# Kernel optimization log

Measured on AMD Instinct MI355X. Metric: run time of the kernel, lower is better.

Reference implementation:

```python
import jax, jax.numpy as jnp
import numpy as np

DIM = 64
N_GRAPHS = 300
N_NODES = 12000
N_EDGES = 40000


def setup_inputs() -> dict:
    key = jax.random.key(0)
    ks = jax.random.split(key, 16)
    N, E, F_IN, D = N_NODES, N_EDGES, 14, DIM

    def w(k, shape, fan_in):
        return jax.random.normal(k, shape, dtype=jnp.float32) / np.float32(np.sqrt(fan_in))

    return {
        "x": jax.random.normal(ks[0], (N, F_IN), dtype=jnp.float32),
        "edge_index": jax.random.randint(ks[1], (2, E), 0, N),
        "edge_attr": jax.random.uniform(ks[2], (E, 4), dtype=jnp.float32),
        "batch": jnp.sort(jax.random.randint(ks[3], (N,), 0, N_GRAPHS)),
        # lin0
        "lin0_w": w(ks[4], (D, F_IN), F_IN), "lin0_b": jnp.zeros((D,), jnp.float32),
        # edge MLP: Linear(4,128) -> ReLU -> Linear(128, D*D)
        "nn1_w": w(ks[5], (128, 4), 4), "nn1_b": jnp.zeros((128,), jnp.float32),
        "nn2_w": w(ks[6], (D * D, 128), 128), "nn2_b": jnp.zeros((D * D,), jnp.float32),
        # NNConv root weight + bias
        "root_w": w(ks[7], (D, D), D), "conv_b": jnp.zeros((D,), jnp.float32),
        # GRU(D, D), gate order r,z,n
        "gru_w_ih": w(ks[8], (3 * D, D), D), "gru_w_hh": w(ks[9], (3 * D, D), D),
        "gru_b_ih": jnp.zeros((3 * D,), jnp.float32), "gru_b_hh": jnp.zeros((3 * D,), jnp.float32),
        # Set2Set LSTM(2D -> D), gate order i,f,g,o
        "lstm_w_ih": w(ks[10], (4 * D, 2 * D), 2 * D), "lstm_w_hh": w(ks[11], (4 * D, D), D),
        "lstm_b_ih": jnp.zeros((4 * D,), jnp.float32), "lstm_b_hh": jnp.zeros((4 * D,), jnp.float32),
        # readout
        "lin1_w": w(ks[12], (D, 2 * D), 2 * D), "lin1_b": jnp.zeros((D,), jnp.float32),
        "lin2_w": w(ks[13], (1, D), D), "lin2_b": jnp.zeros((1,), jnp.float32),
    }


def _mpnn_forward(x, edge_index, edge_attr, batch,
                  lin0_w, lin0_b, nn1_w, nn1_b, nn2_w, nn2_b, root_w, conv_b,
                  gru_w_ih, gru_w_hh, gru_b_ih, gru_b_hh,
                  lstm_w_ih, lstm_w_hh, lstm_b_ih, lstm_b_hh,
                  lin1_w, lin1_b, lin2_w, lin2_b):
    N, D, B = x.shape[0], DIM, N_GRAPHS
    src, dst = edge_index[0], edge_index[1]

    out = jax.nn.relu(x @ lin0_w.T + lin0_b)          # [N, D]
    h = out

    # per-edge weight matrices from edge MLP: [E, D, D]
    W_e = (jax.nn.relu(edge_attr @ nn1_w.T + nn1_b) @ nn2_w.T + nn2_b).reshape(-1, D, D)
    deg = jnp.maximum(
        jax.ops.segment_sum(jnp.ones(src.shape, x.dtype), dst, num_segments=N), 1.0)

    for _ in range(3):
        # NNConv: gather -> per-edge bmm -> scatter-mean, plus root term and bias
        msg = jnp.einsum('ei,eio->eo', out[src], W_e)                 # [E, D]
        agg = jax.ops.segment_sum(msg, dst, num_segments=N) / deg[:, None]
        m = jax.nn.relu(out @ root_w + agg + conv_b)
        # GRU cell (torch gate order r, z, n)
        gx = m @ gru_w_ih.T + gru_b_ih
        gh = h @ gru_w_hh.T + gru_b_hh
        r = jax.nn.sigmoid(gx[:, :D] + gh[:, :D])
        z = jax.nn.sigmoid(gx[:, D:2 * D] + gh[:, D:2 * D])
        n = jnp.tanh(gx[:, 2 * D:] + r * gh[:, 2 * D:])
        h = (1.0 - z) * n + z * h
        out = h

    per_atom_out = out

    # Set2Set pooling, 3 processing steps
    q_star = jnp.zeros((B, 2 * D), x.dtype)
    hs = jnp.zeros((B, D), x.dtype)
    cs = jnp.zeros((B, D), x.dtype)
    for _ in range(3):
        gates = q_star @ lstm_w_ih.T + lstm_b_ih + hs @ lstm_w_hh.T + lstm_b_hh
        i_g = jax.nn.sigmoid(gates[:, 0 * D:1 * D])
        f_g = jax.nn.sigmoid(gates[:, 1 * D:2 * D])
        g_g = jnp.tanh(gates[:, 2 * D:3 * D])
        o_g = jax.nn.sigmoid(gates[:, 3 * D:4 * D])
        cs = f_g * cs + i_g * g_g
        hs = o_g * jnp.tanh(cs)
        q = hs                                                         # [B, D]
        e = jnp.sum(out * q[batch], axis=-1)                           # [N]
        e_max = jax.ops.segment_max(e, batch, num_segments=B)
        a = jnp.exp(e - e_max[batch])
        a = a / jax.ops.segment_sum(a, batch, num_segments=B)[batch]   # scatter-softmax
        r_read = jax.ops.segment_sum(a[:, None] * out, batch, num_segments=B)
        q_star = jnp.concatenate([q, r_read], axis=-1)                 # [B, 2D]

    y = jax.nn.relu(q_star @ lin1_w.T + lin1_b)
    y = (y @ lin2_w.T + lin2_b).reshape(-1)                            # [B]
    return (y, per_atom_out)


def reference(x, edge_index, edge_attr, batch,
              lin0_w, lin0_b, nn1_w, nn1_b, nn2_w, nn2_b, root_w, conv_b,
              gru_w_ih, gru_w_hh, gru_b_ih, gru_b_hh,
              lstm_w_ih, lstm_w_hh, lstm_b_ih, lstm_b_hh,
              lin1_w, lin1_b, lin2_w, lin2_b):
    return _mpnn_forward(x, edge_index, edge_attr, batch,
                         lin0_w, lin0_b, nn1_w, nn1_b, nn2_w, nn2_b, root_w, conv_b,
                         gru_w_ih, gru_w_hh, gru_b_ih, gru_b_hh,
                         lstm_w_ih, lstm_w_hh, lstm_b_ih, lstm_b_hh,
                         lin1_w, lin1_b, lin2_w, lin2_b)
```

## Files before the change

kernel.cpp:

```cpp
#include <hip/hip_runtime.h>
#include <math.h>

#define NBG 300
#define KP 8256

typedef __attribute__((ext_vector_type(8))) short short8_t;
typedef __attribute__((ext_vector_type(4))) float f32x4_t;

#define MFMA16(a,b,c) __builtin_amdgcn_mfma_f32_16x16x32_bf16(a,b,c,0,0,0)

__device__ __forceinline__ float sigmoidf_(float x){ return 1.0f/(1.0f+expf(-x)); }
__device__ __forceinline__ float bf2f(short s){
  union{unsigned u; float f;} v; v.u = ((unsigned)(unsigned short)s) << 16; return v.f;
}
__device__ __forceinline__ short f2bf(float f){
  union{float f; unsigned u;} v; v.f = f;
  unsigned r = (v.u + 0x7fffu + ((v.u >> 16) & 1u)) >> 16;
  return (short)r;
}
__device__ __forceinline__ unsigned cvt_pk_bf16(float lo, float hi){
  unsigned r;
  asm volatile("v_cvt_pk_bf16_f32 %0, %1, %2" : "=v"(r) : "v"(lo), "v"(hi));
  return r;
}
union FragA { short8_t v; unsigned u[4]; };

__device__ __forceinline__ short8_t frag_from(float sv, short8_t h){
  union { short8_t v; unsigned u[4]; } hh; hh.v = h;
  FragA fa;
  #pragma unroll
  for (int k2 = 0; k2 < 4; ++k2){
    float lo = __uint_as_float(hh.u[k2] << 16);
    float hi = __uint_as_float(hh.u[k2] & 0xffff0000u);
    fa.u[k2] = cvt_pk_bf16(sv*lo, sv*hi);
  }
  return fa.v;
}

__global__ void lin0_kernel(const float* __restrict__ x, const float* __restrict__ w,
                            const float* __restrict__ b, float* __restrict__ out,
                            short* __restrict__ out_bf, int N){
  int n = blockIdx.x; int d = threadIdx.x;
  __shared__ float xs[16];
  if (d < 14) xs[d] = x[n*14 + d];
  __syncthreads();
  float acc = b[d];
  #pragma unroll
  for (int k = 0; k < 14; ++k) acc = fmaf(xs[k], w[d*14 + k], acc);
  float v = fmaxf(acc, 0.0f);
  out[n*64 + d] = v;
  out_bf[n*64 + d] = f2bf(v);
}

__global__ void ehid_kernel(const float* __restrict__ ea, const float* __restrict__ w,
                            const float* __restrict__ b, short* __restrict__ hid_bf, int E){
  int e = blockIdx.x; int t = threadIdx.x;
  __shared__ float as[4];
  if (t < 4) as[t] = ea[e*4 + t];
  __syncthreads();
  float acc = b[t];
  #pragma unroll
  for (int k = 0; k < 4; ++k) acc = fmaf(as[k], w[t*4 + k], acc);
  hid_bf[(size_t)e*128 + t] = f2bf(fmaxf(acc, 0.0f));
}

__global__ void count_kernel(const int* __restrict__ idx, int* __restrict__ counts, int len){
  int e = blockIdx.x*blockDim.x + threadIdx.x;
  if (e < len) atomicAdd(&counts[idx[e]], 1);
}

__global__ __launch_bounds__(1024) void scan_kernel(const int* __restrict__ counts,
    int* __restrict__ starts, int* __restrict__ cursor, int N){
  __shared__ int part[1024];
  int t = threadIdx.x;
  int per = (N + 1023) >> 10;
  int base = t * per;
  int s = 0;
  for (int j = 0; j < per; ++j){ int idx = base + j; if (idx < N) s += counts[idx]; }
  part[t] = s;
  __syncthreads();
  for (int off = 1; off < 1024; off <<= 1){
    int v = (t >= off) ? part[t - off] : 0;
    __syncthreads();
    part[t] += v;
    __syncthreads();
  }
  int run = (t == 0) ? 0 : part[t-1];
  for (int j = 0; j < per; ++j){
    int idx = base + j;
    if (idx < N){ starts[idx] = run; cursor[idx] = run; run += counts[idx]; }
  }
}

__global__ void scatter_kernel(const int* __restrict__ dst, int* __restrict__ cursor,
                               int* __restrict__ sorted_eid, int E){
  int e = blockIdx.x*blockDim.x + threadIdx.x;
  if (e < E){ int p = atomicAdd(&cursor[dst[e]], 1); sorted_eid[p] = e; }
}

__global__ void w2t_build(const float* __restrict__ w2, const float* __restrict__ b2,
                          short* __restrict__ W2t){
  int o = blockIdx.x;
  for (int k = threadIdx.x; k < KP; k += blockDim.x){
    float val;
    if (k < 8192){ int i = k >> 7, h = k & 127; val = w2[(size_t)(i*64 + o)*128 + h]; }
    else val = b2[(k - 8192)*64 + o];
    W2t[(size_t)o*KP + k] = f2bf(val);
  }
}

__global__ __launch_bounds__(256) void msg_gemm3(
    const short* __restrict__ out_bf, const short* __restrict__ hid_bf,
    const short* __restrict__ W2t, const int* __restrict__ sorted,
    const int* __restrict__ src, const int* __restrict__ dstv,
    float* __restrict__ agg, int E)
{
  __shared__ short sSb[128*80];
  __shared__ __align__(16) char bufB[4][4096];
  __shared__ int eid_s[128];
  __shared__ int dst_s[128];

  const int tid = threadIdx.x;
  const int blk = blockIdx.x;
  const int split = blockIdx.y;

  if (tid < 128){
    int p = blk*128 + tid;
    int e = (p < E) ? sorted[p] : -1;
    eid_s[tid] = e;
    dst_s[tid] = (e >= 0) ? dstv[e] : -1;
  }
  __syncthreads();

  const int lane = tid & 63, wid = tid >> 6;
  const int r = lane & 15, q4 = lane >> 4;
  const int eloc0 = wid*32 + r;
  const int eloc1 = eloc0 + 16;

  short8_t z8 = {0,0,0,0,0,0,0,0};

  {
    int row = tid >> 1, half = tid & 1;
    int e = eid_s[row];
    short* dp = sSb + row*80 + half*32;
    if (e >= 0){
      const short* sp = out_bf + (size_t)src[e]*64 + half*32;
      *(short8_t*)(dp)      = *(const short8_t*)(sp);
      *(short8_t*)(dp + 8)  = *(const short8_t*)(sp + 8);
      *(short8_t*)(dp + 16) = *(const short8_t*)(sp + 16);
      *(short8_t*)(dp + 24) = *(const short8_t*)(sp + 24);
    } else {
      *(short8_t*)(dp) = z8; *(short8_t*)(dp + 8) = z8;
      *(short8_t*)(dp + 16) = z8; *(short8_t*)(dp + 24) = z8;
    }
  }

  short8_t hq0_0=z8, hq0_1=z8, hq0_2=z8, hq0_3=z8;
  short8_t hq1_0=z8, hq1_1=z8, hq1_2=z8, hq1_3=z8;
  {
    int e0 = eid_s[eloc0], e1 = eid_s[eloc1];
    if (e0 >= 0){
      const short* hp = hid_bf + (size_t)e0*128 + q4*8;
      hq0_0 = *(const short8_t*)(hp);      hq0_1 = *(const short8_t*)(hp + 32);
      hq0_2 = *(const short8_t*)(hp + 64); hq0_3 = *(const short8_t*)(hp + 96);
    }
    if (e1 >= 0){
      const short* hp = hid_bf + (size_t)e1*128 + q4*8;
      hq1_0 = *(const short8_t*)(hp);      hq1_1 = *(const short8_t*)(hp + 32);
      hq1_2 = *(const short8_t*)(hp + 64); hq1_3 = *(const short8_t*)(hp + 96);
    }
  }

  const int gl_o  = tid >> 2;
  const int gl_kq = (tid & 3) ^ ((tid >> 3) & 3);
  const char* w2b = (const char*)W2t;
  const size_t gbase = (size_t)gl_o*(KP*2) + (size_t)gl_kq*16;

  int boff0, boff1, boff2, boff3;
  {
    int o0 = r, o1 = 16 + r, o2 = 32 + r, o3 = 48 + r;
    boff0 = (o0*4 + (q4 ^ ((o0 >> 1) & 3))) * 16;
    boff1 = (o1*4 + (q4 ^ ((o1 >> 1) & 3))) * 16;
    boff2 = (o2*4 + (q4 ^ ((o2 >> 1) & 3))) * 16;
    boff3 = (o3*4 + (q4 ^ ((o3 >> 1) & 3))) * 16;
  }

  const int nc     = split ? 130 : 128;
  const int cstart = split * 128;
  const int clast  = cstart + nc - 1;

#define GLOAD(c_, bi_)                                                          \
  __builtin_amdgcn_global_load_lds(                                             \
      (const __attribute__((address_space(1))) unsigned*)(w2b + gbase + (size_t)(c_)*64), \
      (__attribute__((address_space(3))) unsigned*)(&bufB[bi_][wid*1024]), 16, 0, 0)

  GLOAD(cstart + 0, (cstart + 0) & 3);
  GLOAD(cstart + 1, (cstart + 1) & 3);
  GLOAD(cstart + 2, (cstart + 2) & 3);
  __syncthreads();

  f32x4_t zz = {0.f,0.f,0.f,0.f};
  f32x4_t acc00 = zz, acc01 = zz, acc02 = zz, acc03 = zz;
  f32x4_t acc10 = zz, acc11 = zz, acc12 = zz, acc13 = zz;

#define CHUNK(QI, Q, HQ0, HQ1)                                                  \
  {                                                                             \
    int c = cstart + (QI)*4 + (Q);                                              \
    asm volatile("s_waitcnt vmcnt(2) lgkmcnt(0)" ::: "memory");                 \
    __builtin_amdgcn_s_barrier();                                               \
    const char* bp = bufB[c & 3];                                               \
    short8_t b0 = *(const short8_t*)(bp + boff0);                               \
    short8_t b1 = *(const short8_t*)(bp + boff1);                               \
    short8_t b2 = *(const short8_t*)(bp + boff2);                               \
    short8_t b3 = *(const short8_t*)(bp + boff3);                               \
    { int cn = c + 3; if (cn > clast) cn = clast; GLOAD(cn, (c + 3) & 3); }     \
    short8_t f0 = frag_from(sv0, HQ0);                                          \
    short8_t f1 = frag_from(sv1, HQ1);                                          \
    acc00 = MFMA16(f0, b0, acc00);                                              \
    acc01 = MFMA16(f0, b1, acc01);                                              \
    acc02 = MFMA16(f0, b2, acc02);                                              \
    acc03 = MFMA16(f0, b3, acc03);                                              \
    acc10 = MFMA16(f1, b0, acc10);                                              \
    acc11 = MFMA16(f1, b1, acc11);                                              \
    acc12 = MFMA16(f1, b2, acc12);                                              \
    acc13 = MFMA16(f1, b3, acc13);                                              \
  }

  #pragma unroll 1
  for (int qi = 0; qi < 32; ++qi){
    int qg = (split << 5) + qi;
    float sv0 = bf2f(sSb[eloc0*80 + qg]);
    float sv1 = bf2f(sSb[eloc1*80 + qg]);
    CHUNK(qi, 0, hq0_0, hq1_0)
    CHUNK(qi, 1, hq0_1, hq1_1)
    CHUNK(qi, 2, hq0_2, hq1_2)
    CHUNK(qi, 3, hq0_3, hq1_3)
  }

  if (split){
    #pragma unroll
    for (int tc = 0; tc < 2; ++tc){
      int c = 256 + tc;
      asm volatile("s_waitcnt vmcnt(2) lgkmcnt(0)" ::: "memory");
      __builtin_amdgcn_s_barrier();
      const char* bp = bufB[c & 3];
      short8_t b0 = *(const short8_t*)(bp + boff0);
      short8_t b1 = *(const short8_t*)(bp + boff1);
      short8_t b2 = *(const short8_t*)(bp + boff2);
      short8_t b3 = *(const short8_t*)(bp + boff3);
      GLOAD(clast, (c + 3) & 3);
      short8_t f0 = *(const short8_t*)(sSb + eloc0*80 + tc*32 + q4*8);
      short8_t f1 = *(const short8_t*)(sSb + eloc1*80 + tc*32 + q4*8);
      acc00 = MFMA16(f0, b0, acc00);
      acc01 = MFMA16(f0, b1, acc01);
      acc02 = MFMA16(f0, b2, acc02);
      acc03 = MFMA16(f0, b3, acc03);
      acc10 = MFMA16(f1, b0, acc10);
      acc11 = MFMA16(f1, b1, acc11);
      acc12 = MFMA16(f1, b2, acc12);
      acc13 = MFMA16(f1, b3, acc13);
    }
  }

  asm volatile("s_waitcnt vmcnt(0)" ::: "memory");

  {
    int ebase = wid*32 + q4*4;
    float c0 = 0.f, c1 = 0.f, c2 = 0.f, c3 = 0.f;
    #pragma unroll
    for (int reg = 0; reg < 4; ++reg){
      c0 += acc00[reg]; c1 += acc01[reg]; c2 += acc02[reg]; c3 += acc03[reg];
      int d = dst_s[ebase + reg];
      int dn = (reg < 3) ? dst_s[ebase + reg + 1] : -2;
      if (d != dn){
        if (d >= 0){
          float* ap = agg + (size_t)d*64;
          atomicAdd(ap + r,      c0);
          atomicAdd(ap + 16 + r, c1);
          atomicAdd(ap + 32 + r, c2);
          atomicAdd(ap + 48 + r, c3);
        }
        c0 = c1 = c2 = c3 = 0.f;
      }
    }
  }
  {
    int ebase = wid*32 + 16 + q4*4;
    float c0 = 0.f, c1 = 0.f, c2 = 0.f, c3 = 0.f;
    #pragma unroll
    for (int reg = 0; reg < 4; ++reg){
      c0 += acc10[reg]; c1 += acc11[reg]; c2 += acc12[reg]; c3 += acc13[reg];
      int d = dst_s[ebase + reg];
      int dn = (reg < 3) ? dst_s[ebase + reg + 1] : -2;
      if (d != dn){
        if (d >= 0){
          float* ap = agg + (size_t)d*64;
          atomicAdd(ap + r,      c0);
          atomicAdd(ap + 16 + r, c1);
          atomicAdd(ap + 32 + r, c2);
          atomicAdd(ap + 48 + r, c3);
        }
        c0 = c1 = c2 = c3 = 0.f;
      }
    }
  }
#undef CHUNK
#undef GLOAD
}

__global__ __launch_bounds__(256) void node_mfma(
    const short* __restrict__ out_bf, const float* __restrict__ agg,
    const int* __restrict__ counts,
    const float* __restrict__ root_w, const float* __restrict__ conv_b,
    const float* __restrict__ gwih, const float* __restrict__ gwhh,
    const float* __restrict__ gbih, const float* __restrict__ gbhh,
    float* __restrict__ out, short* __restrict__ out_bf_w,
    float* __restrict__ out_dup, int N)
{
  __shared__ short XH[64*128];
  __shared__ short rootT[64*64];
  __shared__ short Wih_s[192*64];
  __shared__ short Whh_s[192*64];
  __shared__ float rdeg_s[64];
  __shared__ float cb_s[64];

  int tid = threadIdx.x;
  int blk = blockIdx.x;
  int nbase = blk*64;

  {
    int n = tid >> 2, cq = tid & 3;
    int ng = nbase + n;
    short8_t v0 = {0,0,0,0,0,0,0,0}, v1 = v0;
    if (ng < N){
      const short* p = out_bf + (size_t)ng*64;
      v0 = *(const short8_t*)(p + cq*16);
      v1 = *(const short8_t*)(p + cq*16 + 8);
    }
    int c0 = 8 + cq*2;
    *(short8_t*)(XH + n*128 + ((c0     ^ (n & 7))*8)) = v0;
    *(short8_t*)(XH + n*128 + (((c0+1) ^ (n & 7))*8)) = v1;
  }
  {
    int i = tid >> 2, dq = tid & 3;
    #pragma unroll
    for (int j = 0; j < 16; ++j){
      int d = dq*16 + j;
      short v = f2bf(root_w[i*64 + d]);
      rootT[d*64 + (((i >> 3) ^ (d & 7))*8) + (i & 7)] = v;
    }
  }
  if (tid < 192){
    int g = tid;
    short pk[8];
    #pragma unroll
    for (int c = 0; c < 8; ++c){
      #pragma unroll
      for (int j = 0; j < 8; ++j) pk[j] = f2bf(gwih[g*64 + c*8 + j]);
      *(short8_t*)(Wih_s + g*64 + ((c ^ (g & 7))*8)) = *(short8_t*)&pk[0];
    }
    #pragma unroll
    for (int c = 0; c < 8; ++c){
      #pragma unroll
      for (int j = 0; j < 8; ++j) pk[j] = f2bf(gwhh[g*64 + c*8 + j]);
      *(short8_t*)(Whh_s + g*64 + ((c ^ (g & 7))*8)) = *(short8_t*)&pk[0];
    }
  }
  if (tid < 64){
    int ng = nbase + tid;
    int c = (ng < N) ? counts[ng] : 1;
    rdeg_s[tid] = 1.0f / fmaxf((float)c, 1.0f);
    cb_s[tid] = conv_b[tid];
  }
  __syncthreads();

  int lane = tid & 63, wid = tid >> 6;
  int r = lane & 15, q4 = lane >> 4;

  {
    int mh = (wid >> 1)*32, nh = (wid & 1)*32;
    f32x4_t z4 = {0.f,0.f,0.f,0.f};
    f32x4_t c00 = z4, c01 = z4, c10 = z4, c11 = z4;
    #pragma unroll
    for (int ks = 0; ks < 2; ++ks){
      int ck = 8 + ks*4 + q4;
      int swA = (ck ^ (r & 7))*8;
      int swB = ((ks*4 + q4) ^ (r & 7))*8;
      short8_t a0 = *(const short8_t*)(XH + (mh + r)*128 + swA);
      short8_t a1 = *(const short8_t*)(XH + (mh + 16 + r)*128 + swA);
      short8_t b0 = *(const short8_t*)(rootT + (nh + r)*64 + swB);
      short8_t b1 = *(const short8_t*)(rootT + (nh + 16 + r)*64 + swB);
      c00 = MFMA16(a0, b0, c00);
      c01 = MFMA16(a0, b1, c01);
      c10 = MFMA16(a1, b0, c10);
      c11 = MFMA16(a1, b1, c11);
    }
    #pragma unroll
    for (int mm = 0; mm < 2; ++mm){
      #pragma unroll
      for (int nn = 0; nn < 2; ++nn){
        f32x4_t cc = mm == 0 ? (nn == 0 ? c00 : c01) : (nn == 0 ? c10 : c11);
        int d = nh + nn*16 + r;
        #pragma unroll
        for (int reg = 0; reg < 4; ++reg){
          int n = mh + mm*16 + q4*4 + reg;
          int ng = nbase + n;
          float av = (ng < N) ? agg[(size_t)ng*64 + d] : 0.0f;
          float v = cc[reg] + av * rdeg_s[n] + cb_s[d];
          v = fmaxf(v, 0.0f);
          XH[n*128 + (((d >> 3) ^ (n & 7))*8) + (d & 7)] = f2bf(v);
        }
      }
    }
  }
  __syncthreads();

  f32x4_t ax[4][3], ah[4][3];
  {
    f32x4_t z4 = {0.f,0.f,0.f,0.f};
    #pragma unroll
    for (int mt = 0; mt < 4; ++mt)
      #pragma unroll
      for (int gt = 0; gt < 3; ++gt){ ax[mt][gt] = z4; ah[mt][gt] = z4; }
  }
  #pragma unroll
  for (int ks = 0; ks < 2; ++ks){
    int ckM = ks*4 + q4;
    int ckH = 8 + ks*4 + q4;
    int swM = (ckM ^ (r & 7))*8;
    int swH = (ckH ^ (r & 7))*8;
    int swB = ((ks*4 + q4) ^ (r & 7))*8;
    short8_t bx[3], bh[3];
    #pragma unroll
    for (int gt = 0; gt < 3; ++gt){
      int g = gt*64 + wid*16 + r;
      bx[gt] = *(const short8_t*)(Wih_s + g*64 + swB);
      bh[gt] = *(const short8_t*)(Whh_s + g*64 + swB);
    }
    #pragma unroll
    for (int mt = 0; mt < 4; ++mt){
      short8_t aM = *(const short8_t*)(XH + (mt*16 + r)*128 + swM);
      short8_t aH = *(const short8_t*)(XH + (mt*16 + r)*128 + swH);
      #pragma unroll
      for (int gt = 0; gt < 3; ++gt){
        ax[mt][gt] = MFMA16(aM, bx[gt], ax[mt][gt]);
        ah[mt][gt] = MFMA16(aH, bh[gt], ah[mt][gt]);
      }
    }
  }

  {
    int d = wid*16 + r;
    float bir = gbih[d],      bhr = gbhh[d];
    float biz = gbih[64 + d], bhz = gbhh[64 + d];
    float bin_ = gbih[128 + d], bhn = gbhh[128 + d];
    #pragma unroll
    for (int mt = 0; mt < 4; ++mt){
      #pragma unroll
      for (int reg = 0; reg < 4; ++reg){
        int n = mt*16 + q4*4 + reg;
        int ng = nbase + n;
        if (ng < N){
          float gxr = ax[mt][0][reg], gxz = ax[mt][1][reg], gxn = ax[mt][2][reg];
          float ghr = ah[mt][0][reg], ghz = ah[mt][1][reg], ghn = ah[mt][2][reg];
          float rr = sigmoidf_(gxr + ghr + bir + bhr);
          float zz = sigmoidf_(gxz + ghz + biz + bhz);
          float nn = tanhf(gxn + bin_ + rr*(ghn + bhn));
          float h = out[(size_t)ng*64 + d];
          float v = (1.0f - zz)*nn + zz*h;
          out[(size_t)ng*64 + d] = v;
          out_bf_w[(size_t)ng*64 + d] = f2bf(v);
          if (out_dup) out_dup[(size_t)ng*64 + d] = v;
        }
      }
    }
  }
}

__global__ __launch_bounds__(256) void set2set_kernel(
    const float* __restrict__ out, const int* __restrict__ bstarts,
    const int* __restrict__ bcounts,
    const float* __restrict__ lwih, const float* __restrict__ lwhh,
    const float* __restrict__ lbih, const float* __restrict__ lbhh,
    const float* __restrict__ l1w, const float* __restrict__ l1b,
    const float* __restrict__ l2w, const float* __restrict__ l2b,
    float* __restrict__ y)
{
  int b = blockIdx.x, t = threadIdx.x;
  int lane = t & 63, wid = t >> 6;
  __shared__ float qs[128];
  __shared__ float hsl[64], hs_s[64], cs_s[64];
  __shared__ float ev[512];
  __shared__ float red[256];
  __shared__ float rpart[4][64];
  __shared__ float scal[2];

  int s0 = bstarts[b], cnt = bcounts[b];
  if (cnt > 512) cnt = 512;
  if (t < 64){ hs_s[t] = 0.f; cs_s[t] = 0.f; }
  if (t < 128) qs[t] = 0.f;
  __syncthreads();

  for (int step = 0; step < 3; ++step){
    if (t < 64) hsl[t] = hs_s[t];
    __syncthreads();
    {
      float a0 = lbih[t] + lbhh[t], a1 = 0.f, a2 = 0.f, a3 = 0.f;
      const float* wi = lwih + t*128;
      #pragma unroll
      for (int kq = 0; kq < 32; ++kq){
        float4 w4 = *(const float4*)(wi + kq*4);
        a0 = fmaf(qs[kq*4+0], w4.x, a0);
        a1 = fmaf(qs[kq*4+1], w4.y, a1);
        a2 = fmaf(qs[kq*4+2], w4.z, a2);
        a3 = fmaf(qs[kq*4+3], w4.w, a3);
      }
      const float* wh = lwhh + t*64;
      #pragma unroll
      for (int kq = 0; kq < 16; ++kq){
        float4 w4 = *(const float4*)(wh + kq*4);
        a0 = fmaf(hsl[kq*4+0], w4.x, a0);
        a1 = fmaf(hsl[kq*4+1], w4.y, a1);
        a2 = fmaf(hsl[kq*4+2], w4.z, a2);
        a3 = fmaf(hsl[kq*4+3], w4.w, a3);
      }
      red[t] = (a0 + a1) + (a2 + a3);
    }
    __syncthreads();
    if (t < 64){
      float ig = sigmoidf_(red[t]);
      float fg = sigmoidf_(red[64 + t]);
      float gg = tanhf(red[128 + t]);
      float og = sigmoidf_(red[192 + t]);
      float c = fg*cs_s[t] + ig*gg;
      cs_s[t] = c;
      hs_s[t] = og*tanhf(c);
    }
    __syncthreads();

    float lmax = -1e30f;
    for (int idx = t; idx < cnt; idx += 256){
      const float* row = out + (size_t)(s0 + idx)*64;
      float a0 = 0.f, a1 = 0.f, a2 = 0.f, a3 = 0.f;
      #pragma unroll
      for (int kq = 0; kq < 16; ++kq){
        float4 v = *(const float4*)(row + kq*4);
        a0 = fmaf(v.x, hs_s[kq*4+0], a0);
        a1 = fmaf(v.y, hs_s[kq*4+1], a1);
        a2 = fmaf(v.z, hs_s[kq*4+2], a2);
        a3 = fmaf(v.w, hs_s[kq*4+3], a3);
      }
      float acc = (a0 + a1) + (a2 + a3);
      ev[idx] = acc;
      lmax = fmaxf(lmax, acc);
    }
    red[t] = lmax;
    __syncthreads();
    #pragma unroll
    for (int off = 128; off > 0; off >>= 1){
      if (t < off) red[t] = fmaxf(red[t], red[t + off]);
      __syncthreads();
    }
    if (t == 0) scal[0] = red[0];
    __syncthreads();
    float m = scal[0];

    float ls = 0.f;
    for (int idx = t; idx < cnt; idx += 256){
      float a = expf(ev[idx] - m);
      ev[idx] = a;
      ls += a;
    }
    red[t] = ls;
    __syncthreads();
    #pragma unroll
    for (int off = 128; off > 0; off >>= 1){
      if (t < off) red[t] += red[t + off];
      __syncthreads();
    }
    if (t == 0) scal[1] = red[0];
    __syncthreads();
    float lst = scal[1];

    float part = 0.f;
    for (int idx = wid; idx < cnt; idx += 4)
      part = fmaf(ev[idx], out[(size_t)(s0 + idx)*64 + lane], part);
    rpart[wid][lane] = part;
    __syncthreads();
    if (t < 64){
      float r = (rpart[0][t] + rpart[1][t]) + (rpart[2][t] + rpart[3][t]);
      r = (cnt > 0) ? r / lst : 0.f;
      qs[t] = hs_s[t];
      qs[64 + t] = r;
    }
    __syncthreads();
  }

  if (t < 64){
    float a0 = l1b[t], a1 = 0.f, a2 = 0.f, a3 = 0.f;
    const float* w1 = l1w + t*128;
    #pragma unroll
    for (int kq = 0; kq < 32; ++kq){
      float4 w4 = *(const float4*)(w1 + kq*4);
      a0 = fmaf(qs[kq*4+0], w4.x, a0);
      a1 = fmaf(qs[kq*4+1], w4.y, a1);
      a2 = fmaf(qs[kq*4+2], w4.z, a2);
      a3 = fmaf(qs[kq*4+3], w4.w, a3);
    }
    float acc = (a0 + a1) + (a2 + a3);
    float v = fmaxf(acc, 0.0f) * l2w[t];
    #pragma unroll
    for (int off = 32; off > 0; off >>= 1) v += __shfl_xor(v, off, 64);
    if (t == 0) y[b] = v + l2b[0];
  }
}

extern "C" void kernel_launch(void* const* d_in, const int* in_sizes, int n_in,
                              void* d_out, int out_size, void* d_ws, size_t ws_size,
                              hipStream_t stream){
  const float* x      = (const float*)d_in[0];
  const int*   ei     = (const int*)  d_in[1];
  const float* ea     = (const float*)d_in[2];
  const int*   batch  = (const int*)  d_in[3];
  const float* lin0_w = (const float*)d_in[4];
  const float* lin0_b = (const float*)d_in[5];
  const float* nn1_w  = (const float*)d_in[6];
  const float* nn1_b  = (const float*)d_in[7];
  const float* nn2_w  = (const float*)d_in[8];
  const float* nn2_b  = (const float*)d_in[9];
  const float* root_w = (const float*)d_in[10];
  const float* conv_b = (const float*)d_in[11];
  const float* gwih   = (const float*)d_in[12];
  const float* gwhh   = (const float*)d_in[13];
  const float* gbih   = (const float*)d_in[14];
  const float* gbhh   = (const float*)d_in[15];
  const float* lwih   = (const float*)d_in[16];
  const float* lwhh   = (const float*)d_in[17];
  const float* lbih   = (const float*)d_in[18];
  const float* lbhh   = (const float*)d_in[19];
  const float* l1w    = (const float*)d_in[20];
  const float* l1b    = (const float*)d_in[21];
  const float* l2w    = (const float*)d_in[22];
  const float* l2b    = (const float*)d_in[23];

  const int N = in_sizes[0] / 14;
  const int E = in_sizes[1] / 2;
  const int B = NBG;
  const int* src  = ei;
  const int* dstv = ei + E;

  char* wsp = (char*)d_ws; size_t off = 0;
  auto alloc = [&](size_t bytes)->char* {
    char* p = wsp + off; off += (bytes + 255) & ~((size_t)255); return p;
  };
  float* out     = (float*)alloc((size_t)N*64*4);
  short* out_bf  = (short*)alloc((size_t)N*64*2);
  float* agg     = (float*)alloc((size_t)N*64*4);
  int*   counts  = (int*)  alloc((size_t)N*4);
  int*   starts  = (int*)  alloc((size_t)N*4);
  int*   cursor  = (int*)  alloc((size_t)N*4);
  int*   sorted  = (int*)  alloc((size_t)E*4);
  int*   bcounts = (int*)  alloc((size_t)B*4);
  int*   bstarts = (int*)  alloc((size_t)B*4);
  int*   bcursor = (int*)  alloc((size_t)B*4);
  short* hid_bf  = (short*)alloc((size_t)E*128*2);
  short* W2t     = (short*)alloc((size_t)64*KP*2);

  lin0_kernel<<<N, 64, 0, stream>>>(x, lin0_w, lin0_b, out, out_bf, N);
  ehid_kernel<<<E, 128, 0, stream>>>(ea, nn1_w, nn1_b, hid_bf, E);

  hipMemsetAsync(counts, 0, (size_t)N*4, stream);
  count_kernel<<<(E + 255)/256, 256, 0, stream>>>(dstv, counts, E);
  scan_kernel<<<1, 1024, 0, stream>>>(counts, starts, cursor, N);
  scatter_kernel<<<(E + 255)/256, 256, 0, stream>>>(dstv, cursor, sorted, E);

  hipMemsetAsync(bcounts, 0, (size_t)B*4, stream);
  count_kernel<<<(N + 255)/256, 256, 0, stream>>>(batch, bcounts, N);
  scan_kernel<<<1, 1024, 0, stream>>>(bcounts, bstarts, bcursor, B);

  w2t_build<<<64, 256, 0, stream>>>(nn2_w, nn2_b, W2t);

  int mblocks = (E + 127)/128;
  int nblocks = (N + 63)/64;
  dim3 mg(mblocks, 2);
  for (int it = 0; it < 3; ++it){
    hipMemsetAsync(agg, 0, (size_t)N*64*4, stream);
    msg_gemm3<<<mg, 256, 0, stream>>>(out_bf, hid_bf, W2t, sorted, src, dstv, agg, E);
    node_mfma<<<nblocks, 256, 0, stream>>>(out_bf, agg, counts, root_w, conv_b,
                                           gwih, gwhh, gbih, gbhh, out, out_bf,
                                           (it == 2) ? ((float*)d_out + 300) : nullptr, N);
  }

  set2set_kernel<<<B, 256, 0, stream>>>(out, bstarts, bcounts, lwih, lwhh, lbih, lbhh,
                                        l1w, l1b, l2w, l2b, (float*)d_out);
}
```

Before: 388.6 us.

## Deepen msg GEMM prefetch pipeline, fuse count/scan launches, zero agg in consumer

The message GEMM now keeps eight LDS stages of W2 tiles instead of four and handles two K-chunks per barrier, which halves the barrier count and keeps more global loads in flight. The A-tile row padding also shrinks from 80 to 72 shorts. The two count kernels and the two scan kernels are each merged into one launch, sharing a single memset over contiguous buffers. The per-iteration agg memset is replaced by node_mfma zeroing agg after it reads it. In exchange, LDS use grows and the wait counts in the tail path depend on the exact prefetch bookkeeping.

```diff
diff --git a/kernel.cpp b/kernel.cpp
--- a/kernel.cpp
+++ b/kernel.cpp
@@ -64,13 +64,22 @@
   hid_bf[(size_t)e*128 + t] = f2bf(fmaxf(acc, 0.0f));
 }
 
-__global__ void count_kernel(const int* __restrict__ idx, int* __restrict__ counts, int len){
-  int e = blockIdx.x*blockDim.x + threadIdx.x;
-  if (e < len) atomicAdd(&counts[idx[e]], 1);
-}
-
-__global__ __launch_bounds__(1024) void scan_kernel(const int* __restrict__ counts,
-    int* __restrict__ starts, int* __restrict__ cursor, int N){
+__global__ void count2_kernel(const int* __restrict__ dstv, int E,
+                              const int* __restrict__ batch, int N,
+                              int* __restrict__ counts, int* __restrict__ bcounts){
+  int i = blockIdx.x*blockDim.x + threadIdx.x;
+  if (i < E) atomicAdd(&counts[dstv[i]], 1);
+  int j = i - E;
+  if (j >= 0 && j < N) atomicAdd(&bcounts[batch[j]], 1);
+}
+
+__global__ __launch_bounds__(1024) void scan2_kernel(
+    const int* __restrict__ countsA, int* __restrict__ startsA, int* __restrict__ cursorA, int NA,
+    const int* __restrict__ countsB, int* __restrict__ startsB, int* __restrict__ cursorB, int NB){
+  const int* counts = blockIdx.x ? countsB : countsA;
+  int* starts = blockIdx.x ? startsB : startsA;
+  int* cursor = blockIdx.x ? cursorB : cursorA;
+  int N = blockIdx.x ? NB : NA;
   __shared__ int part[1024];
   int t = threadIdx.x;
   int per = (N + 1023) >> 10;
@@ -109,14 +118,14 @@
   }
 }
 
-__global__ __launch_bounds__(256) void msg_gemm3(
+__global__ __launch_bounds__(256) void msg_gemm4(
     const short* __restrict__ out_bf, const short* __restrict__ hid_bf,
     const short* __restrict__ W2t, const int* __restrict__ sorted,
     const int* __restrict__ src, const int* __restrict__ dstv,
     float* __restrict__ agg, int E)
 {
-  __shared__ short sSb[128*80];
-  __shared__ __align__(16) char bufB[4][4096];
+  __shared__ short sSb[128*72];
+  __shared__ __align__(16) char bufB[8][4096];
   __shared__ int eid_s[128];
   __shared__ int dst_s[128];
 
@@ -142,7 +151,7 @@
   {
     int row = tid >> 1, half = tid & 1;
     int e = eid_s[row];
-    short* dp = sSb + row*80 + half*32;
+    short* dp = sSb + row*72 + half*32;
     if (e >= 0){
       const short* sp = out_bf + (size_t)src[e]*64 + half*32;
       *(short8_t*)(dp)      = *(const short8_t*)(sp);
@@ -194,72 +203,95 @@
       (const __attribute__((address_space(1))) unsigned*)(w2b + gbase + (size_t)(c_)*64), \
       (__attribute__((address_space(3))) unsigned*)(&bufB[bi_][wid*1024]), 16, 0, 0)
 
-  GLOAD(cstart + 0, (cstart + 0) & 3);
-  GLOAD(cstart + 1, (cstart + 1) & 3);
-  GLOAD(cstart + 2, (cstart + 2) & 3);
-  __syncthreads();
+  GLOAD(cstart + 0, 0); GLOAD(cstart + 1, 1); GLOAD(cstart + 2, 2);
+  GLOAD(cstart + 3, 3); GLOAD(cstart + 4, 4); GLOAD(cstart + 5, 5);
+  asm volatile("s_waitcnt lgkmcnt(0)" ::: "memory");
+  __builtin_amdgcn_s_barrier();
 
   f32x4_t zz = {0.f,0.f,0.f,0.f};
   f32x4_t acc00 = zz, acc01 = zz, acc02 = zz, acc03 = zz;
   f32x4_t acc10 = zz, acc11 = zz, acc12 = zz, acc13 = zz;
 
-#define CHUNK(QI, Q, HQ0, HQ1)                                                  \
+#define PHASE(P, HA0, HA1, HB0, HB1)                                            \
   {                                                                             \
-    int c = cstart + (QI)*4 + (Q);                                              \
-    asm volatile("s_waitcnt vmcnt(2) lgkmcnt(0)" ::: "memory");                 \
+    int ca = cstart + 2*(P), cb = ca + 1;                                       \
+    asm volatile("s_waitcnt vmcnt(4) lgkmcnt(0)" ::: "memory");                 \
     __builtin_amdgcn_s_barrier();                                               \
-    const char* bp = bufB[c & 3];                                               \
-    short8_t b0 = *(const short8_t*)(bp + boff0);                               \
-    short8_t b1 = *(const short8_t*)(bp + boff1);                               \
-    short8_t b2 = *(const short8_t*)(bp + boff2);                               \
-    short8_t b3 = *(const short8_t*)(bp + boff3);                               \
-    { int cn = c + 3; if (cn > clast) cn = clast; GLOAD(cn, (c + 3) & 3); }     \
-    short8_t f0 = frag_from(sv0, HQ0);                                          \
-    short8_t f1 = frag_from(sv1, HQ1);                                          \
-    acc00 = MFMA16(f0, b0, acc00);                                              \
-    acc01 = MFMA16(f0, b1, acc01);                                              \
-    acc02 = MFMA16(f0, b2, acc02);                                              \
-    acc03 = MFMA16(f0, b3, acc03);                                              \
-    acc10 = MFMA16(f1, b0, acc10);                                              \
-    acc11 = MFMA16(f1, b1, acc11);                                              \
-    acc12 = MFMA16(f1, b2, acc12);                                              \
-    acc13 = MFMA16(f1, b3, acc13);                                              \
+    { int c6 = ca + 6; if (c6 > clast) c6 = clast; GLOAD(c6, (ca + 6) & 7); }   \
+    { int c7 = cb + 6; if (c7 > clast) c7 = clast; GLOAD(c7, (cb + 6) & 7); }   \
+    const char* bpa = bufB[ca & 7];                                             \
+    const char* bpb = bufB[cb & 7];                                             \
+    short8_t bA0 = *(const short8_t*)(bpa + boff0);                             \
+    short8_t bA1 = *(const short8_t*)(bpa + boff1);                             \
+    short8_t bA2 = *(const short8_t*)(bpa + boff2);                             \
+    short8_t bA3 = *(const short8_t*)(bpa + boff3);                             \
+    short8_t bB0 = *(const short8_t*)(bpb + boff0);                             \
+    short8_t bB1 = *(const short8_t*)(bpb + boff1);                             \
+    short8_t bB2 = *(const short8_t*)(bpb + boff2);                             \
+    short8_t bB3 = *(const short8_t*)(bpb + boff3);                             \
+    short8_t fA0 = frag_from(sv0, HA0);                                         \
+    short8_t fA1 = frag_from(sv1, HA1);                                         \
+    acc00 = MFMA16(fA0, bA0, acc00);                                            \
+    acc01 = MFMA16(fA0, bA1, acc01);                                            \
+    acc02 = MFMA16(fA0, bA2, acc02);                                            \
+    acc03 = MFMA16(fA0, bA3, acc03);                                            \
+    acc10 = MFMA16(fA1, bA0, acc10);                                            \
+    acc11 = MFMA16(fA1, bA1, acc11);                                            \
+    acc12 = MFMA16(fA1, bA2, acc12);                                            \
+    acc13 = MFMA16(fA1, bA3, acc13);                                            \
+    short8_t fB0 = frag_from(sv0, HB0);                                         \
+    short8_t fB1 = frag_from(sv1, HB1);                                         \
+    acc00 = MFMA16(fB0, bB0, acc00);                                            \
+    acc01 = MFMA16(fB0, bB1, acc01);                                            \
+    acc02 = MFMA16(fB0, bB2, acc02);                                            \
+    acc03 = MFMA16(fB0, bB3, acc03);                                            \
+    acc10 = MFMA16(fB1, bB0, acc10);                                            \
+    acc11 = MFMA16(fB1, bB1, acc11);                                            \
+    acc12 = MFMA16(fB1, bB2, acc12);                                            \
+    acc13 = MFMA16(fB1, bB3, acc13);                                            \
   }
 
   #pragma unroll 1
   for (int qi = 0; qi < 32; ++qi){
-    int qg = (split << 5) + qi;
-    float sv0 = bf2f(sSb[eloc0*80 + qg]);
-    float sv1 = bf2f(sSb[eloc1*80 + qg]);
-    CHUNK(qi, 0, hq0_0, hq1_0)
-    CHUNK(qi, 1, hq0_1, hq1_1)
-    CHUNK(qi, 2, hq0_2, hq1_2)
-    CHUNK(qi, 3, hq0_3, hq1_3)
+    float sv0 = bf2f(sSb[eloc0*72 + (split << 5) + qi]);
+    float sv1 = bf2f(sSb[eloc1*72 + (split << 5) + qi]);
+    PHASE(qi*2,     hq0_0, hq1_0, hq0_1, hq1_1)
+    PHASE(qi*2 + 1, hq0_2, hq1_2, hq0_3, hq1_3)
   }
 
   if (split){
-    #pragma unroll
-    for (int tc = 0; tc < 2; ++tc){
-      int c = 256 + tc;
-      asm volatile("s_waitcnt vmcnt(2) lgkmcnt(0)" ::: "memory");
-      __builtin_amdgcn_s_barrier();
-      const char* bp = bufB[c & 3];
-      short8_t b0 = *(const short8_t*)(bp + boff0);
-      short8_t b1 = *(const short8_t*)(bp + boff1);
-      short8_t b2 = *(const short8_t*)(bp + boff2);
-      short8_t b3 = *(const short8_t*)(bp + boff3);
-      GLOAD(clast, (c + 3) & 3);
-      short8_t f0 = *(const short8_t*)(sSb + eloc0*80 + tc*32 + q4*8);
-      short8_t f1 = *(const short8_t*)(sSb + eloc1*80 + tc*32 + q4*8);
-      acc00 = MFMA16(f0, b0, acc00);
-      acc01 = MFMA16(f0, b1, acc01);
-      acc02 = MFMA16(f0, b2, acc02);
-      acc03 = MFMA16(f0, b3, acc03);
-      acc10 = MFMA16(f1, b0, acc10);
-      acc11 = MFMA16(f1, b1, acc11);
-      acc12 = MFMA16(f1, b2, acc12);
-      acc13 = MFMA16(f1, b3, acc13);
-    }
+    asm volatile("s_waitcnt vmcnt(4) lgkmcnt(0)" ::: "memory");
+    __builtin_amdgcn_s_barrier();
+    const char* bpa = bufB[0];
+    const char* bpb = bufB[1];
+    short8_t bA0 = *(const short8_t*)(bpa + boff0);
+    short8_t bA1 = *(const short8_t*)(bpa + boff1);
+    short8_t bA2 = *(const short8_t*)(bpa + boff2);
+    short8_t bA3 = *(const short8_t*)(bpa + boff3);
+    short8_t bB0 = *(const short8_t*)(bpb + boff0);
+    short8_t bB1 = *(const short8_t*)(bpb + boff1);
+    short8_t bB2 = *(const short8_t*)(bpb + boff2);
+    short8_t bB3 = *(const short8_t*)(bpb + boff3);
+    short8_t fA0 = *(const short8_t*)(sSb + eloc0*72 + q4*8);
+    short8_t fA1 = *(const short8_t*)(sSb + eloc1*72 + q4*8);
+    short8_t fB0 = *(const short8_t*)(sSb + eloc0*72 + 32 + q4*8);
+    short8_t fB1 = *(const short8_t*)(sSb + eloc1*72 + 32 + q4*8);
+    acc00 = MFMA16(fA0, bA0, acc00);
+    acc01 = MFMA16(fA0, bA1, acc01);
+    acc02 = MFMA16(fA0, bA2, acc02);
+    acc03 = MFMA16(fA0, bA3, acc03);
+    acc10 = MFMA16(fA1, bA0, acc10);
+    acc11 = MFMA16(fA1, bA1, acc11);
+    acc12 = MFMA16(fA1, bA2, acc12);
+    acc13 = MFMA16(fA1, bA3, acc13);
+    acc00 = MFMA16(fB0, bB0, acc00);
+    acc01 = MFMA16(fB0, bB1, acc01);
+    acc02 = MFMA16(fB0, bB2, acc02);
+    acc03 = MFMA16(fB0, bB3, acc03);
+    acc10 = MFMA16(fB1, bB0, acc10);
+    acc11 = MFMA16(fB1, bB1, acc11);
+    acc12 = MFMA16(fB1, bB2, acc12);
+    acc13 = MFMA16(fB1, bB3, acc13);
   }
 
   asm volatile("s_waitcnt vmcnt(0)" ::: "memory");
@@ -304,12 +336,12 @@
       }
     }
   }
-#undef CHUNK
+#undef PHASE
 #undef GLOAD
 }
 
 __global__ __launch_bounds__(256) void node_mfma(
-    const short* __restrict__ out_bf, const float* __restrict__ agg,
+    const short* __restrict__ out_bf, float* __restrict__ agg,
     const int* __restrict__ counts,
     const float* __restrict__ root_w, const float* __restrict__ conv_b,
     const float* __restrict__ gwih, const float* __restrict__ gwhh,
@@ -405,7 +437,11 @@
         for (int reg = 0; reg < 4; ++reg){
           int n = mh + mm*16 + q4*4 + reg;
           int ng = nbase + n;
-          float av = (ng < N) ? agg[(size_t)ng*64 + d] : 0.0f;
+          float av = 0.0f;
+          if (ng < N){
+            av = agg[(size_t)ng*64 + d];
+            agg[(size_t)ng*64 + d] = 0.0f;
+          }
           float v = cc[reg] + av * rdeg_s[n] + cb_s[d];
           v = fmaxf(v, 0.0f);
           XH[n*128 + (((d >> 3) ^ (n & 7))*8) + (d & 7)] = f2bf(v);
@@ -657,10 +693,10 @@
   short* out_bf  = (short*)alloc((size_t)N*64*2);
   float* agg     = (float*)alloc((size_t)N*64*4);
   int*   counts  = (int*)  alloc((size_t)N*4);
+  int*   bcounts = (int*)  alloc((size_t)B*4);
   int*   starts  = (int*)  alloc((size_t)N*4);
   int*   cursor  = (int*)  alloc((size_t)N*4);
   int*   sorted  = (int*)  alloc((size_t)E*4);
-  int*   bcounts = (int*)  alloc((size_t)B*4);
   int*   bstarts = (int*)  alloc((size_t)B*4);
   int*   bcursor = (int*)  alloc((size_t)B*4);
   short* hid_bf  = (short*)alloc((size_t)E*128*2);
@@ -669,23 +705,21 @@
   lin0_kernel<<<N, 64, 0, stream>>>(x, lin0_w, lin0_b, out, out_bf, N);
   ehid_kernel<<<E, 128, 0, stream>>>(ea, nn1_w, nn1_b, hid_bf, E);
 
-  hipMemsetAsync(counts, 0, (size_t)N*4, stream);
-  count_kernel<<<(E + 255)/256, 256, 0, stream>>>(dstv, counts, E);
-  scan_kernel<<<1, 1024, 0, stream>>>(counts, starts, cursor, N);
+  size_t cspan = (((size_t)N*4 + 255) & ~(size_t)255) + (size_t)B*4;
+  hipMemsetAsync(counts, 0, cspan, stream);
+  count2_kernel<<<(E + N + 255)/256, 256, 0, stream>>>(dstv, E, batch, N, counts, bcounts);
+  scan2_kernel<<<2, 1024, 0, stream>>>(counts, starts, cursor, N,
+                                       bcounts, bstarts, bcursor, B);
   scatter_kernel<<<(E + 255)/256, 256, 0, stream>>>(dstv, cursor, sorted, E);
 
-  hipMemsetAsync(bcounts, 0, (size_t)B*4, stream);
-  count_kernel<<<(N + 255)/256, 256, 0, stream>>>(batch, bcounts, N);
-  scan_kernel<<<1, 1024, 0, stream>>>(bcounts, bstarts, bcursor, B);
-
   w2t_build<<<64, 256, 0, stream>>>(nn2_w, nn2_b, W2t);
+  hipMemsetAsync(agg, 0, (size_t)N*64*4, stream);
 
   int mblocks = (E + 127)/128;
   int nblocks = (N + 63)/64;
   dim3 mg(mblocks, 2);
   for (int it = 0; it < 3; ++it){
-    hipMemsetAsync(agg, 0, (size_t)N*64*4, stream);
-    msg_gemm3<<<mg, 256, 0, stream>>>(out_bf, hid_bf, W2t, sorted, src, dstv, agg, E);
+    msg_gemm4<<<mg, 256, 0, stream>>>(out_bf, hid_bf, W2t, sorted, src, dstv, agg, E);
     node_mfma<<<nblocks, 256, 0, stream>>>(out_bf, agg, counts, root_w, conv_b,
                                            gwih, gwhh, gbih, gbhh, out, out_bf,
                                            (it == 2) ? ((float*)d_out + 300) : nullptr, N);
```

Result: slower. 409.8 us (+5.5%).

## Split message GEMM K-range four ways, fuse count/scan kernels, zero agg in node kernel

Applied to the files above, without the earlier changes.

The message GEMM grid now splits the K dimension into four slices instead of two, so each block handles 64 chunks and twice as many blocks run, at the cost of more atomic adds into agg. The edge and batch count kernels are merged into one launch, and the two scans run as one two-block launch, which removes several small launches and memsets. The per-iteration agg memset is dropped: node_mfma now zeroes agg after reading it, and a single memset before the loop initialises it. Together these aim to cut launch overhead and raise occupancy of the dominant GEMM.

```diff
diff --git a/kernel.cpp b/kernel.cpp
--- a/kernel.cpp
+++ b/kernel.cpp
@@ -64,13 +64,22 @@
   hid_bf[(size_t)e*128 + t] = f2bf(fmaxf(acc, 0.0f));
 }
 
-__global__ void count_kernel(const int* __restrict__ idx, int* __restrict__ counts, int len){
-  int e = blockIdx.x*blockDim.x + threadIdx.x;
-  if (e < len) atomicAdd(&counts[idx[e]], 1);
-}
-
-__global__ __launch_bounds__(1024) void scan_kernel(const int* __restrict__ counts,
-    int* __restrict__ starts, int* __restrict__ cursor, int N){
+__global__ void count2_kernel(const int* __restrict__ dstv, int E,
+                              const int* __restrict__ batch, int N,
+                              int* __restrict__ counts, int* __restrict__ bcounts){
+  int i = blockIdx.x*blockDim.x + threadIdx.x;
+  if (i < E) atomicAdd(&counts[dstv[i]], 1);
+  int j = i - E;
+  if (j >= 0 && j < N) atomicAdd(&bcounts[batch[j]], 1);
+}
+
+__global__ __launch_bounds__(1024) void scan2_kernel(
+    const int* __restrict__ countsA, int* __restrict__ startsA, int* __restrict__ cursorA, int NA,
+    const int* __restrict__ countsB, int* __restrict__ startsB, int* __restrict__ cursorB, int NB){
+  const int* counts = blockIdx.x ? countsB : countsA;
+  int* starts = blockIdx.x ? startsB : startsA;
+  int* cursor = blockIdx.x ? cursorB : cursorA;
+  int N = blockIdx.x ? NB : NA;
   __shared__ int part[1024];
   int t = threadIdx.x;
   int per = (N + 1023) >> 10;
@@ -185,8 +194,9 @@
     boff3 = (o3*4 + (q4 ^ ((o3 >> 1) & 3))) * 16;
   }
 
-  const int nc     = split ? 130 : 128;
-  const int cstart = split * 128;
+  const bool last  = (split == 3);
+  const int cstart = split * 64;
+  const int nc     = last ? 66 : 64;
   const int clast  = cstart + nc - 1;
 
 #define GLOAD(c_, bi_)                                                          \
@@ -227,8 +237,8 @@
   }
 
   #pragma unroll 1
-  for (int qi = 0; qi < 32; ++qi){
-    int qg = (split << 5) + qi;
+  for (int qi = 0; qi < 16; ++qi){
+    int qg = (split << 4) + qi;
     float sv0 = bf2f(sSb[eloc0*80 + qg]);
     float sv1 = bf2f(sSb[eloc1*80 + qg]);
     CHUNK(qi, 0, hq0_0, hq1_0)
@@ -237,8 +247,8 @@
     CHUNK(qi, 3, hq0_3, hq1_3)
   }
 
-  if (split){
-    #pragma unroll
+  if (last){
+    #pragma unroll 1
     for (int tc = 0; tc < 2; ++tc){
       int c = 256 + tc;
       asm volatile("s_waitcnt vmcnt(2) lgkmcnt(0)" ::: "memory");
@@ -309,7 +319,7 @@
 }
 
 __global__ __launch_bounds__(256) void node_mfma(
-    const short* __restrict__ out_bf, const float* __restrict__ agg,
+    const short* __restrict__ out_bf, float* __restrict__ agg,
     const int* __restrict__ counts,
     const float* __restrict__ root_w, const float* __restrict__ conv_b,
     const float* __restrict__ gwih, const float* __restrict__ gwhh,
@@ -405,7 +415,11 @@
         for (int reg = 0; reg < 4; ++reg){
           int n = mh + mm*16 + q4*4 + reg;
           int ng = nbase + n;
-          float av = (ng < N) ? agg[(size_t)ng*64 + d] : 0.0f;
+          float av = 0.0f;
+          if (ng < N){
+            av = agg[(size_t)ng*64 + d];
+            agg[(size_t)ng*64 + d] = 0.0f;
+          }
           float v = cc[reg] + av * rdeg_s[n] + cb_s[d];
           v = fmaxf(v, 0.0f);
           XH[n*128 + (((d >> 3) ^ (n & 7))*8) + (d & 7)] = f2bf(v);
@@ -657,10 +671,10 @@
   short* out_bf  = (short*)alloc((size_t)N*64*2);
   float* agg     = (float*)alloc((size_t)N*64*4);
   int*   counts  = (int*)  alloc((size_t)N*4);
+  int*   bcounts = (int*)  alloc((size_t)B*4);
   int*   starts  = (int*)  alloc((size_t)N*4);
   int*   cursor  = (int*)  alloc((size_t)N*4);
   int*   sorted  = (int*)  alloc((size_t)E*4);
-  int*   bcounts = (int*)  alloc((size_t)B*4);
   int*   bstarts = (int*)  alloc((size_t)B*4);
   int*   bcursor = (int*)  alloc((size_t)B*4);
   short* hid_bf  = (short*)alloc((size_t)E*128*2);
@@ -669,22 +683,20 @@
   lin0_kernel<<<N, 64, 0, stream>>>(x, lin0_w, lin0_b, out, out_bf, N);
   ehid_kernel<<<E, 128, 0, stream>>>(ea, nn1_w, nn1_b, hid_bf, E);
 
-  hipMemsetAsync(counts, 0, (size_t)N*4, stream);
-  count_kernel<<<(E + 255)/256, 256, 0, stream>>>(dstv, counts, E);
-  scan_kernel<<<1, 1024, 0, stream>>>(counts, starts, cursor, N);
+  size_t cspan = (((size_t)N*4 + 255) & ~(size_t)255) + (size_t)B*4;
+  hipMemsetAsync(counts, 0, cspan, stream);
+  count2_kernel<<<(E + N + 255)/256, 256, 0, stream>>>(dstv, E, batch, N, counts, bcounts);
+  scan2_kernel<<<2, 1024, 0, stream>>>(counts, starts, cursor, N,
+                                       bcounts, bstarts, bcursor, B);
   scatter_kernel<<<(E + 255)/256, 256, 0, stream>>>(dstv, cursor, sorted, E);
 
-  hipMemsetAsync(bcounts, 0, (size_t)B*4, stream);
-  count_kernel<<<(N + 255)/256, 256, 0, stream>>>(batch, bcounts, N);
-  scan_kernel<<<1, 1024, 0, stream>>>(bcounts, bstarts, bcursor, B);
-
   w2t_build<<<64, 256, 0, stream>>>(nn2_w, nn2_b, W2t);
+  hipMemsetAsync(agg, 0, (size_t)N*64*4, stream);
 
   int mblocks = (E + 127)/128;
   int nblocks = (N + 63)/64;
-  dim3 mg(mblocks, 2);
+  dim3 mg(mblocks, 4);
   for (int it = 0; it < 3; ++it){
-    hipMemsetAsync(agg, 0, (size_t)N*64*4, stream);
     msg_gemm3<<<mg, 256, 0, stream>>>(out_bf, hid_bf, W2t, sorted, src, dstv, agg, E);
     node_mfma<<<nblocks, 256, 0, stream>>>(out_bf, agg, counts, root_w, conv_b,
                                            gwih, gwhh, gbih, gbhh, out, out_bf,
```

Result: faster. 353.0 us (median of 2 runs) (-9.1%).
